# Optimization experiments

Hardware: AMD Instinct MI355X
Metric: run time of the kernel (lower is better)

Reference implementation:

```python
import jax, jax.numpy as jnp
import numpy as np

NUM_EMBEDDINGS = 4096
EMBEDDING_DIM = 256


def setup_inputs() -> dict:
    key = jax.random.key(0)
    k1, k2 = jax.random.split(key)
    # x: [B, C, H, W] latent feature map, C == embedding_dim
    x = jax.random.normal(k1, (4, EMBEDDING_DIM, 64, 64), dtype=jnp.float32)
    # codebook initialized uniform(-1/K, 1/K) as in the torch module
    emb = jax.random.uniform(
        k2, (NUM_EMBEDDINGS, EMBEDDING_DIM), dtype=jnp.float32,
        minval=-1.0 / NUM_EMBEDDINGS, maxval=1.0 / NUM_EMBEDDINGS)
    return {"x": x, "emb": emb}


def reference(x, emb):
    # x: [B, C, H, W] -> x_flat: [B, L, C] with L = H*W
    B, C = x.shape[0], x.shape[1]
    x_flat = x.reshape(B, C, -1).transpose(0, 2, 1)
    x_sq = jnp.sum(x_flat * x_flat, axis=2, keepdims=True)      # [B, L, 1]
    e_sq = jnp.sum(emb * emb, axis=1)                            # [K]
    dots = jnp.einsum('blc,kc->blk', x_flat, emb)                # [B, L, K]
    distances = x_sq + e_sq - 2.0 * dots
    closest_indices = jnp.argmin(distances, axis=2)              # [B, L]
    return closest_indices, distances
```

## Files before the change

kernel.cpp:

```cpp
#include <hip/hip_runtime.h>
#include <hip/hip_fp16.h>

#define BB 4
#define CC 256
#define LL 4096
#define MM 16384
#define KK 4096
#define MARGIN 1.0e-4f

typedef _Float16 half8 __attribute__((ext_vector_type(8)));
typedef _Float16 half4_ __attribute__((ext_vector_type(4)));
typedef float f32x4 __attribute__((ext_vector_type(4)));

#define GLOAD16(gp, lp) __builtin_amdgcn_global_load_lds( \
    (const __attribute__((address_space(1))) void*)(gp),  \
    (__attribute__((address_space(3))) void*)(lp), 16, 0, 0)

__global__ void vq_prep_x(const float* __restrict__ x,
                          _Float16* __restrict__ xh, float* __restrict__ xsq) {
  __shared__ float tl[32][260];
  const int b = blockIdx.y, l0 = blockIdx.x * 32;
  const int t = threadIdx.x;
  const float* src = x + (size_t)b * CC * LL + l0;

#pragma unroll
  for (int it = 0; it < 32; ++it) {
    const int idx = it * 256 + t;
    const int c = idx >> 5, l = idx & 31;
    tl[l][c] = src[(size_t)c * LL + l];
  }
  __syncthreads();

#pragma unroll
  for (int it = 0; it < 4; ++it) {
    const int u = it * 256 + t;
    const int l = u >> 5, c8 = (u & 31) * 8;
    half8 h;
#pragma unroll
    for (int j = 0; j < 8; ++j) h[j] = (_Float16)tl[l][c8 + j];
    *(half8*)(xh + ((size_t)(b * LL + l0 + l)) * CC + c8) = h;
  }

  if (t < 32) {
    float S[2];
#pragma unroll
    for (int blk = 0; blk < 2; ++blk) {
      float v[16];
#pragma unroll
      for (int ln = 0; ln < 16; ++ln) {
        float q[8];
#pragma unroll
        for (int j = 0; j < 8; ++j) {
          const float xv = tl[t][blk * 128 + j * 16 + ln];
          q[j] = xv * xv;
        }
        v[ln] = ((q[0] + q[1]) + (q[2] + q[3])) + ((q[4] + q[5]) + (q[6] + q[7]));
      }
      float s1[8], s2[4], s3[2];
#pragma unroll
      for (int ln = 0; ln < 8; ++ln) s1[ln] = v[ln] + v[ln + 8];
#pragma unroll
      for (int ln = 0; ln < 4; ++ln) s2[ln] = s1[ln] + s1[ln + 4];
#pragma unroll
      for (int ln = 0; ln < 2; ++ln) s3[ln] = s2[ln] + s2[ln + 2];
      S[blk] = s3[0] + s3[1];
    }
    xsq[b * LL + l0 + t] = S[0] + S[1];
  }
}

__global__ void vq_esq_np(const float* __restrict__ emb, float* __restrict__ esq) {
  const int q = blockIdx.x * 256 + threadIdx.x;
  const float* pe = emb + (size_t)q * CC;
  float S[2];
#pragma unroll
  for (int blk = 0; blk < 2; ++blk) {
    float v[16];
#pragma unroll
    for (int ln = 0; ln < 16; ++ln) {
      float qq[8];
#pragma unroll
      for (int j = 0; j < 8; ++j) {
        float ev = pe[blk * 128 + j * 16 + ln];
        qq[j] = ev * ev;
      }
      v[ln] = ((qq[0] + qq[1]) + (qq[2] + qq[3])) + ((qq[4] + qq[5]) + (qq[6] + qq[7]));
    }
    float s1[8], s2[4], s3[2];
#pragma unroll
    for (int ln = 0; ln < 8; ++ln) s1[ln] = v[ln] + v[ln + 8];
#pragma unroll
    for (int ln = 0; ln < 4; ++ln) s2[ln] = s1[ln] + s1[ln + 4];
#pragma unroll
    for (int ln = 0; ln < 2; ++ln) s3[ln] = s2[ln] + s2[ln + 2];
    S[blk] = s3[0] + s3[1];
  }
  esq[q] = S[0] + S[1];
}

__global__ void vq_split_e(const float* __restrict__ emb, _Float16* __restrict__ eh) {
  const int lane = threadIdx.x & 63, wid = threadIdx.x >> 6;
  const int q = blockIdx.x * 4 + wid;
  const float4 v = ((const float4*)(emb + (size_t)q * CC))[lane];
  float vv[4] = {v.x, v.y, v.z, v.w};
  _Float16 h[4];
#pragma unroll
  for (int i = 0; i < 4; ++i) h[i] = (_Float16)(vv[i] * 4096.0f);
  *(half4_*)(eh + (size_t)q * CC + lane * 4) = half4_{h[0], h[1], h[2], h[3]};
}

__global__ __launch_bounds__(256) void vq_gemm(
    const _Float16* __restrict__ xh, const _Float16* __restrict__ eh,
    const float* __restrict__ xsq, const float* __restrict__ esq,
    float* __restrict__ out,
    float* __restrict__ ps1, int* __restrict__ pi1, float* __restrict__ ps2) {
  __shared__ __align__(16) char smem[32768];
  _Float16* sAb[2] = {(_Float16*)smem, (_Float16*)(smem + 16384)};
  _Float16* sBb[2] = {(_Float16*)(smem + 8192), (_Float16*)(smem + 24576)};
  float* sOut = (float*)smem;

  const int t = threadIdx.x, lane = t & 63, wid = t >> 6;
  const int wm = wid >> 1, wn = wid & 1;
  const int m0 = blockIdx.x * 128, n0 = blockIdx.y * 128;
  const int lm = lane & 15, kb = lane >> 4;

  const int srow = lane >> 2;
  const int scol = (lane & 3) * 8;
  const int chunk0 = wid * 2, chunk1 = wid * 2 + 1;
  const int row0 = chunk0 * 16 + srow, row1 = chunk1 * 16 + srow;

  float ev[4], xs4[4][4];
#pragma unroll
  for (int ni = 0; ni < 4; ++ni) ev[ni] = esq[n0 + wn * 64 + ni * 16 + lm];
#pragma unroll
  for (int mi = 0; mi < 4; ++mi)
#pragma unroll
    for (int r = 0; r < 4; ++r)
      xs4[mi][r] = xsq[m0 + wm * 64 + mi * 16 + kb * 4 + r];
  __builtin_amdgcn_sched_barrier(0);

#define STAGE(ks, buf) do {                                                   \
    const int kc_ = (ks) * 32 + scol;                                         \
    GLOAD16(xh + (size_t)(m0 + row0) * CC + kc_, sAb[buf] + chunk0 * 512);    \
    GLOAD16(eh + (size_t)(n0 + row0) * CC + kc_, sBb[buf] + chunk0 * 512);    \
    GLOAD16(xh + (size_t)(m0 + row1) * CC + kc_, sAb[buf] + chunk1 * 512);    \
    GLOAD16(eh + (size_t)(n0 + row1) * CC + kc_, sBb[buf] + chunk1 * 512);    \
  } while (0)

  f32x4 acc[4][4] = {};
  STAGE(0, 0);
#pragma unroll
  for (int ks = 0; ks < 8; ++ks) {
    const int cur = ks & 1;
    if (ks < 7) {
      STAGE(ks + 1, cur ^ 1);
      asm volatile("s_waitcnt vmcnt(4)" ::: "memory");
    } else {
      asm volatile("s_waitcnt vmcnt(0)" ::: "memory");
    }
    __builtin_amdgcn_s_barrier();
    __builtin_amdgcn_sched_barrier(0);

    half8 a[4], bfr[4];
#pragma unroll
    for (int i = 0; i < 4; ++i) {
      a[i]   = *(const half8*)&sAb[cur][(wm * 64 + i * 16 + lm) * 32 + kb * 8];
      bfr[i] = *(const half8*)&sBb[cur][(wn * 64 + i * 16 + lm) * 32 + kb * 8];
    }
#pragma unroll
    for (int mi = 0; mi < 4; ++mi)
#pragma unroll
      for (int ni = 0; ni < 4; ++ni)
        acc[mi][ni] = __builtin_amdgcn_mfma_f32_16x16x32_f16(a[mi], bfr[ni], acc[mi][ni], 0, 0, 0);

    asm volatile("s_waitcnt lgkmcnt(0)" ::: "memory");
    __builtin_amdgcn_s_barrier();
    __builtin_amdgcn_sched_barrier(0);
  }
#undef STAGE

  const int swz = kb << 4;
  const int erow = t >> 3, ej = t & 7;
  const int esw = ((erow >> 2) & 3) << 4;
  const int egm0 = m0 + (erow >> 4) * 64 + (erow & 15);

#pragma unroll
  for (int mi = 0; mi < 4; ++mi) {
    if (mi) __syncthreads();
#pragma unroll
    for (int r = 0; r < 4; ++r) {
      const int row = wm * 16 + kb * 4 + r;
#pragma unroll
      for (int ni = 0; ni < 4; ++ni) {
        float t1 = xs4[mi][r] + ev[ni];
        float d = t1 - acc[mi][ni][r] * 4.8828125e-4f;
        sOut[row * 128 + ((wn * 64 + ni * 16 + lm) ^ swz)] = d;
      }
    }
    __syncthreads();
    float s1 = 3.4e38f, s2 = 3.4e38f;
    int q1 = 0x7fffffff;
    const int gm = egm0 + mi * 16;
#pragma unroll
    for (int i = 0; i < 4; ++i) {
      const int c = 4 * ej + 32 * i;
      const f32x4 v = *(const f32x4*)&sOut[erow * 128 + (c ^ esw)];
      __builtin_nontemporal_store(v, (f32x4*)(out + MM + (size_t)gm * (size_t)KK + n0 + c));
#pragma unroll
      for (int e = 0; e < 4; ++e) {
        const float d = v[e];
        const int q = n0 + c + e;
        if (d < s1 || (d == s1 && q < q1)) { s2 = s1; s1 = d; q1 = q; }
        else s2 = fminf(s2, d);
      }
    }
#pragma unroll
    for (int off = 1; off < 8; off <<= 1) {
      float o1 = __shfl_xor(s1, off), o2 = __shfl_xor(s2, off);
      int oq = __shfl_xor(q1, off);
      float mx = fmaxf(s1, o1);
      if (o1 < s1 || (o1 == s1 && oq < q1)) { s1 = o1; q1 = oq; }
      s2 = fminf(fminf(s2, o2), mx);
    }
    if (ej == 0) {
      const size_t pidx = (size_t)gm * 32 + blockIdx.y;
      ps1[pidx] = s1; pi1[pidx] = q1; ps2[pidx] = s2;
    }
  }
}

__global__ void vq_finish(const float* __restrict__ ps1, const int* __restrict__ pi1,
                          const float* __restrict__ ps2, const float* __restrict__ dist,
                          const float* __restrict__ x, const float* __restrict__ emb,
                          const float* __restrict__ xsq, const float* __restrict__ esq,
                          float* __restrict__ out) {
  __shared__ float xr[4][CC];
  __shared__ int cq[4][64];
  __shared__ int cnt[4];
  const int lane = threadIdx.x & 63, w = threadIdx.x >> 6;
  const int m = blockIdx.x * 4 + w;

  float s1 = 3.4e38f, s2 = 3.4e38f;
  int q1 = 0x7fffffff;
  if (lane < 32) {
    const size_t base = (size_t)m * 32 + lane;
    s1 = ps1[base]; s2 = ps2[base]; q1 = pi1[base];
  }
#pragma unroll
  for (int off = 1; off < 32; off <<= 1) {
    float o1 = __shfl_xor(s1, off), o2 = __shfl_xor(s2, off);
    int oq = __shfl_xor(q1, off);
    float mx = fmaxf(s1, o1);
    if (o1 < s1 || (o1 == s1 && oq < q1)) { s1 = o1; q1 = oq; }
    s2 = fminf(fminf(s2, o2), mx);
  }
  s1 = __shfl(s1, 0); s2 = __shfl(s2, 0); q1 = __shfl(q1, 0);

  if (s2 - s1 > MARGIN) {
    if (lane == 0) out[m] = (float)q1;
    return;
  }

  const int b = m >> 12, l = m & 4095;
#pragma unroll
  for (int j = 0; j < 4; ++j)
    xr[w][lane * 4 + j] = x[((size_t)b * CC + lane * 4 + j) * LL + l];
  if (lane == 0) cnt[w] = 0;

  const float thr = s1 + MARGIN;
  const float4* d4 = (const float4*)(dist + (size_t)m * KK);
  for (int i = 0; i < 16; ++i) {
    float4 v = d4[i * 64 + lane];
    float vv[4] = {v.x, v.y, v.z, v.w};
#pragma unroll
    for (int e = 0; e < 4; ++e)
      if (vv[e] <= thr) {
        int slot = atomicAdd(&cnt[w], 1);
        if (slot < 64) cq[w][slot] = (i * 64 + lane) * 4 + e;
      }
  }
  const int nc = min(cnt[w], 64);
  float bs = 3.4e38f;
  int bq = 0x7fffffff;
  if (lane < nc) {
    const int q = cq[w][lane];
    const float* e = emb + (size_t)q * CC;
    float a = 0.f;
    for (int c = 0; c < CC; ++c) a = fmaf(xr[w][c], e[c], a);
    float t1 = xsq[m] + esq[q];
    bs = t1 - 2.0f * a;
    bq = q;
  }
#pragma unroll
  for (int off = 1; off < 64; off <<= 1) {
    float os = __shfl_xor(bs, off);
    int oq = __shfl_xor(bq, off);
    if (os < bs || (os == bs && oq < bq)) { bs = os; bq = oq; }
  }
  if (lane == 0) out[m] = (float)bq;
}

extern "C" void kernel_launch(void* const* d_in, const int* in_sizes, int n_in,
                              void* d_out, int out_size, void* d_ws, size_t ws_size,
                              hipStream_t stream) {
  const float* x = (const float*)d_in[0];
  const float* emb = (const float*)d_in[1];
  float* out = (float*)d_out;
  char* ws = (char*)d_ws;

  _Float16* xh = (_Float16*)(ws + 0);
  _Float16* eh = (_Float16*)(ws + 8388608);
  float* xsq = (float*)(ws + 10485760);
  float* esq = (float*)(ws + 10551296);
  float* ps1 = (float*)(ws + 10567680);
  int*   pi1 = (int*)(ws + 12664832);
  float* ps2 = (float*)(ws + 14761984);

  vq_prep_x<<<dim3(128, 4), 256, 0, stream>>>(x, xh, xsq);
  vq_esq_np<<<16, 256, 0, stream>>>(emb, esq);
  vq_split_e<<<1024, 256, 0, stream>>>(emb, eh);
  vq_gemm<<<dim3(128, 32), 256, 0, stream>>>(xh, eh, xsq, esq, out, ps1, pi1, ps2);
  vq_finish<<<4096, 256, 0, stream>>>(ps1, pi1, ps2, out + MM, x, emb, xsq, esq, out);
}
```

Measured before the change: 147.4 us.

## Swap MFMA operands to write distances directly from registers, skip LDS epilogue

The GEMM now computes the transposed tile (codebook as A, x as B), so each lane holds four consecutive codebook distances for one row. That lets it store float4 distance rows straight from accumulators and drop the LDS staging, the epilogue barriers and the final-iteration barrier. Partial argmin/second-min results now come in 64 per row instead of 32, and vq_finish reduces all 64 lanes. The two codebook prep kernels are merged into one launch. Direct stores are less coalesced (16-byte pieces per lane spread across rows), and the partial-result workspace doubles.

Result: slower. 177.9 us (+20.7%).

```diff
diff --git a/kernel.cpp b/kernel.cpp
--- a/kernel.cpp
+++ b/kernel.cpp
@@ -69,44 +69,44 @@
   }
 }
 
-__global__ void vq_esq_np(const float* __restrict__ emb, float* __restrict__ esq) {
-  const int q = blockIdx.x * 256 + threadIdx.x;
-  const float* pe = emb + (size_t)q * CC;
-  float S[2];
-#pragma unroll
-  for (int blk = 0; blk < 2; ++blk) {
-    float v[16];
-#pragma unroll
-    for (int ln = 0; ln < 16; ++ln) {
-      float qq[8];
-#pragma unroll
-      for (int j = 0; j < 8; ++j) {
-        float ev = pe[blk * 128 + j * 16 + ln];
-        qq[j] = ev * ev;
-      }
-      v[ln] = ((qq[0] + qq[1]) + (qq[2] + qq[3])) + ((qq[4] + qq[5]) + (qq[6] + qq[7]));
-    }
-    float s1[8], s2[4], s3[2];
-#pragma unroll
-    for (int ln = 0; ln < 8; ++ln) s1[ln] = v[ln] + v[ln + 8];
-#pragma unroll
-    for (int ln = 0; ln < 4; ++ln) s2[ln] = s1[ln] + s1[ln + 4];
-#pragma unroll
-    for (int ln = 0; ln < 2; ++ln) s3[ln] = s2[ln] + s2[ln + 2];
-    S[blk] = s3[0] + s3[1];
-  }
-  esq[q] = S[0] + S[1];
-}
-
-__global__ void vq_split_e(const float* __restrict__ emb, _Float16* __restrict__ eh) {
-  const int lane = threadIdx.x & 63, wid = threadIdx.x >> 6;
-  const int q = blockIdx.x * 4 + wid;
+__global__ void vq_prep_e(const float* __restrict__ emb,
+                          _Float16* __restrict__ eh, float* __restrict__ esq) {
+  const int lane = threadIdx.x & 63, w = threadIdx.x >> 6;
+  const int q = blockIdx.x * 4 + w;
   const float4 v = ((const float4*)(emb + (size_t)q * CC))[lane];
   float vv[4] = {v.x, v.y, v.z, v.w};
   _Float16 h[4];
 #pragma unroll
   for (int i = 0; i < 4; ++i) h[i] = (_Float16)(vv[i] * 4096.0f);
   *(half4_*)(eh + (size_t)q * CC + lane * 4) = half4_{h[0], h[1], h[2], h[3]};
+
+  if (lane == 0) {
+    const float* pe = emb + (size_t)q * CC;
+    float S[2];
+#pragma unroll
+    for (int blk = 0; blk < 2; ++blk) {
+      float vt[16];
+#pragma unroll
+      for (int ln = 0; ln < 16; ++ln) {
+        float qq[8];
+#pragma unroll
+        for (int j = 0; j < 8; ++j) {
+          const float ev = pe[blk * 128 + j * 16 + ln];
+          qq[j] = ev * ev;
+        }
+        vt[ln] = ((qq[0] + qq[1]) + (qq[2] + qq[3])) + ((qq[4] + qq[5]) + (qq[6] + qq[7]));
+      }
+      float s1[8], s2[4], s3[2];
+#pragma unroll
+      for (int ln = 0; ln < 8; ++ln) s1[ln] = vt[ln] + vt[ln + 8];
+#pragma unroll
+      for (int ln = 0; ln < 4; ++ln) s2[ln] = s1[ln] + s1[ln + 4];
+#pragma unroll
+      for (int ln = 0; ln < 2; ++ln) s3[ln] = s2[ln] + s2[ln + 2];
+      S[blk] = s3[0] + s3[1];
+    }
+    esq[q] = S[0] + S[1];
+  }
 }
 
 __global__ __launch_bounds__(256) void vq_gemm(
@@ -117,7 +117,6 @@
   __shared__ __align__(16) char smem[32768];
   _Float16* sAb[2] = {(_Float16*)smem, (_Float16*)(smem + 16384)};
   _Float16* sBb[2] = {(_Float16*)(smem + 8192), (_Float16*)(smem + 24576)};
-  float* sOut = (float*)smem;
 
   const int t = threadIdx.x, lane = t & 63, wid = t >> 6;
   const int wm = wid >> 1, wn = wid & 1;
@@ -129,14 +128,15 @@
   const int chunk0 = wid * 2, chunk1 = wid * 2 + 1;
   const int row0 = chunk0 * 16 + srow, row1 = chunk1 * 16 + srow;
 
-  float ev[4], xs4[4][4];
-#pragma unroll
-  for (int ni = 0; ni < 4; ++ni) ev[ni] = esq[n0 + wn * 64 + ni * 16 + lm];
+  float ev[4][4], xs[4];
 #pragma unroll
   for (int mi = 0; mi < 4; ++mi)
 #pragma unroll
     for (int r = 0; r < 4; ++r)
-      xs4[mi][r] = xsq[m0 + wm * 64 + mi * 16 + kb * 4 + r];
+      ev[mi][r] = esq[n0 + wn * 64 + mi * 16 + kb * 4 + r];
+#pragma unroll
+  for (int ni = 0; ni < 4; ++ni)
+    xs[ni] = xsq[m0 + wm * 64 + ni * 16 + lm];
   __builtin_amdgcn_sched_barrier(0);
 
 #define STAGE(ks, buf) do {                                                   \
@@ -161,69 +161,61 @@
     __builtin_amdgcn_s_barrier();
     __builtin_amdgcn_sched_barrier(0);
 
-    half8 a[4], bfr[4];
+    half8 ef[4], xf[4];
 #pragma unroll
     for (int i = 0; i < 4; ++i) {
-      a[i]   = *(const half8*)&sAb[cur][(wm * 64 + i * 16 + lm) * 32 + kb * 8];
-      bfr[i] = *(const half8*)&sBb[cur][(wn * 64 + i * 16 + lm) * 32 + kb * 8];
+      ef[i] = *(const half8*)&sBb[cur][(wn * 64 + i * 16 + lm) * 32 + kb * 8];
+      xf[i] = *(const half8*)&sAb[cur][(wm * 64 + i * 16 + lm) * 32 + kb * 8];
     }
 #pragma unroll
     for (int mi = 0; mi < 4; ++mi)
 #pragma unroll
       for (int ni = 0; ni < 4; ++ni)
-        acc[mi][ni] = __builtin_amdgcn_mfma_f32_16x16x32_f16(a[mi], bfr[ni], acc[mi][ni], 0, 0, 0);
-
-    asm volatile("s_waitcnt lgkmcnt(0)" ::: "memory");
-    __builtin_amdgcn_s_barrier();
-    __builtin_amdgcn_sched_barrier(0);
+        acc[mi][ni] = __builtin_amdgcn_mfma_f32_16x16x32_f16(ef[mi], xf[ni], acc[mi][ni], 0, 0, 0);
+
+    if (ks < 7) {
+      asm volatile("s_waitcnt lgkmcnt(0)" ::: "memory");
+      __builtin_amdgcn_s_barrier();
+      __builtin_amdgcn_sched_barrier(0);
+    }
   }
 #undef STAGE
 
-  const int swz = kb << 4;
-  const int erow = t >> 3, ej = t & 7;
-  const int esw = ((erow >> 2) & 3) << 4;
-  const int egm0 = m0 + (erow >> 4) * 64 + (erow & 15);
-
-#pragma unroll
-  for (int mi = 0; mi < 4; ++mi) {
-    if (mi) __syncthreads();
-#pragma unroll
-    for (int r = 0; r < 4; ++r) {
-      const int row = wm * 16 + kb * 4 + r;
-#pragma unroll
-      for (int ni = 0; ni < 4; ++ni) {
-        float t1 = xs4[mi][r] + ev[ni];
-        float d = t1 - acc[mi][ni][r] * 4.8828125e-4f;
-        sOut[row * 128 + ((wn * 64 + ni * 16 + lm) ^ swz)] = d;
-      }
-    }
-    __syncthreads();
+  const int by2 = blockIdx.y * 2 + wn;
+#pragma unroll
+  for (int ni = 0; ni < 4; ++ni) {
+    const int m = m0 + wm * 64 + ni * 16 + lm;
+    float* rowp = out + MM + (size_t)m * KK + n0 + wn * 64 + kb * 4;
     float s1 = 3.4e38f, s2 = 3.4e38f;
     int q1 = 0x7fffffff;
-    const int gm = egm0 + mi * 16;
-#pragma unroll
-    for (int i = 0; i < 4; ++i) {
-      const int c = 4 * ej + 32 * i;
-      const f32x4 v = *(const f32x4*)&sOut[erow * 128 + (c ^ esw)];
-      __builtin_nontemporal_store(v, (f32x4*)(out + MM + (size_t)gm * (size_t)KK + n0 + c));
-#pragma unroll
-      for (int e = 0; e < 4; ++e) {
-        const float d = v[e];
-        const int q = n0 + c + e;
+#pragma unroll
+    for (int mi = 0; mi < 4; ++mi) {
+      f32x4 dv;
+#pragma unroll
+      for (int r = 0; r < 4; ++r) {
+        const float t1 = xs[ni] + ev[mi][r];
+        dv[r] = t1 - acc[mi][ni][r] * 4.8828125e-4f;
+      }
+      *(f32x4*)(rowp + mi * 16) = dv;
+      const int qb = n0 + wn * 64 + mi * 16 + kb * 4;
+#pragma unroll
+      for (int r = 0; r < 4; ++r) {
+        const float d = dv[r];
+        const int q = qb + r;
         if (d < s1 || (d == s1 && q < q1)) { s2 = s1; s1 = d; q1 = q; }
         else s2 = fminf(s2, d);
       }
     }
 #pragma unroll
-    for (int off = 1; off < 8; off <<= 1) {
+    for (int off = 16; off < 64; off <<= 1) {
       float o1 = __shfl_xor(s1, off), o2 = __shfl_xor(s2, off);
       int oq = __shfl_xor(q1, off);
       float mx = fmaxf(s1, o1);
       if (o1 < s1 || (o1 == s1 && oq < q1)) { s1 = o1; q1 = oq; }
       s2 = fminf(fminf(s2, o2), mx);
     }
-    if (ej == 0) {
-      const size_t pidx = (size_t)gm * 32 + blockIdx.y;
+    if (kb == 0) {
+      const size_t pidx = (size_t)m * 64 + by2;
       ps1[pidx] = s1; pi1[pidx] = q1; ps2[pidx] = s2;
     }
   }
@@ -240,21 +232,17 @@
   const int lane = threadIdx.x & 63, w = threadIdx.x >> 6;
   const int m = blockIdx.x * 4 + w;
 
-  float s1 = 3.4e38f, s2 = 3.4e38f;
-  int q1 = 0x7fffffff;
-  if (lane < 32) {
-    const size_t base = (size_t)m * 32 + lane;
-    s1 = ps1[base]; s2 = ps2[base]; q1 = pi1[base];
-  }
-#pragma unroll
-  for (int off = 1; off < 32; off <<= 1) {
+  const size_t base = (size_t)m * 64 + lane;
+  float s1 = ps1[base], s2 = ps2[base];
+  int q1 = pi1[base];
+#pragma unroll
+  for (int off = 1; off < 64; off <<= 1) {
     float o1 = __shfl_xor(s1, off), o2 = __shfl_xor(s2, off);
     int oq = __shfl_xor(q1, off);
     float mx = fmaxf(s1, o1);
     if (o1 < s1 || (o1 == s1 && oq < q1)) { s1 = o1; q1 = oq; }
     s2 = fminf(fminf(s2, o2), mx);
   }
-  s1 = __shfl(s1, 0); s2 = __shfl(s2, 0); q1 = __shfl(q1, 0);
 
   if (s2 - s1 > MARGIN) {
     if (lane == 0) out[m] = (float)q1;
@@ -313,12 +301,11 @@
   float* xsq = (float*)(ws + 10485760);
   float* esq = (float*)(ws + 10551296);
   float* ps1 = (float*)(ws + 10567680);
-  int*   pi1 = (int*)(ws + 12664832);
-  float* ps2 = (float*)(ws + 14761984);
+  int*   pi1 = (int*)(ws + 14761984);
+  float* ps2 = (float*)(ws + 18956288);
 
   vq_prep_x<<<dim3(128, 4), 256, 0, stream>>>(x, xh, xsq);
-  vq_esq_np<<<16, 256, 0, stream>>>(emb, esq);
-  vq_split_e<<<1024, 256, 0, stream>>>(emb, eh);
+  vq_prep_e<<<1024, 256, 0, stream>>>(emb, eh, esq);
   vq_gemm<<<dim3(128, 32), 256, 0, stream>>>(xh, eh, xsq, esq, out, ps1, pi1, ps2);
   vq_finish<<<4096, 256, 0, stream>>>(ps1, pi1, ps2, out + MM, x, emb, xsq, esq, out);
 }
```
